# Kernel optimization log

Hardware: AMD Instinct MI355X
Metric: run time of the kernel (lower is better)

The kernel has to match this reference:

```python
import jax, jax.numpy as jnp
import numpy as np

ALPHA = 0.9

def setup_inputs() -> dict:
    key = jax.random.key(0)
    inputs = jax.random.normal(key, (8, 4096, 1024), dtype=jnp.float32)
    return {"inputs": inputs}

def reference(inputs) -> jnp.ndarray:
    # FOFE: y_t = alpha * y_{t-1} + x_t, y_{-1} = 0, over time axis (axis=1, batch_first).
    # Linear recurrence with constant decay -> associative scan over pairs (a, b)
    # representing y -> a*y + b.
    x = inputs  # [B, T, D]
    a = jnp.full(x.shape, ALPHA, dtype=x.dtype)  # decay per step

    def combine(c1, c2):
        a1, b1 = c1
        a2, b2 = c2
        return (a1 * a2, b1 * a2 + b2)

    _, y = jax.lax.associative_scan(combine, (a, x), axis=1)
    return y  # [B, T, D]
```

## Files before the change

### kernel.cpp

```cpp
#include <hip/hip_runtime.h>


#define ALPHA 0.9f
#define T_DIM 4096
#define D_DIM 1024
#define CH    512
#define WARM  128
#define DB    256

__global__ __launch_bounds__(256)
void fofe_kernel(const float* __restrict__ x, float* __restrict__ y) {
    const int NDB = D_DIM / DB;
    const int NCH = T_DIM / CH;

    int blk = blockIdx.x;
    int db  = blk % NDB;
    int ch  = (blk / NDB) % NCH;
    int b   = blk / (NDB * NCH);

    int d  = db * DB + threadIdx.x;
    int t0 = ch * CH;
    int tstart = (t0 >= WARM) ? (t0 - WARM) : 0;

    const float* __restrict__ xp = x + ((size_t)b * T_DIM) * D_DIM + d;
    float*       __restrict__ yp = y + ((size_t)b * T_DIM) * D_DIM + d;

    float acc = 0.0f;

    #pragma unroll 16
    for (int t = tstart; t < t0; ++t) {
        acc = fmaf(acc, ALPHA, xp[(size_t)t * D_DIM]);
    }

    #pragma unroll 16
    for (int t = t0; t < t0 + CH; ++t) {
        acc = fmaf(acc, ALPHA, xp[(size_t)t * D_DIM]);
        yp[(size_t)t * D_DIM] = acc;
    }
}

extern "C" void kernel_launch(void* const* d_in, const int* in_sizes, int n_in,
                              void* d_out, int out_size, void* d_ws, size_t ws_size,
                              hipStream_t stream) {
    const float* x = (const float*)d_in[0];
    float* y = (float*)d_out;

    const int B = 8;
    const int grid = B * (T_DIM / CH) * (D_DIM / DB);
    fofe_kernel<<<grid, DB, 0, stream>>>(x, y);
}
```

Before: 53.74 us.

## Vectorize FOFE scan with float4 per thread and shorten chunks and warmup

Each thread now processes four adjacent channels with float4 loads and stores, and each block covers the full feature width. The time chunk shrinks from 512 to 128 steps and the warmup from 128 to 64 steps. The aim is more bytes in flight per thread and more independent recurrence chains. In exchange, the redundant warmup reads grow as a fraction of chunk length, and the shorter warmup leaves a truncation error of about 0.9^64 that may be near tolerance.

```diff
diff --git a/kernel.cpp b/kernel.cpp
--- a/kernel.cpp
+++ b/kernel.cpp
@@ -4,48 +4,54 @@
 #define ALPHA 0.9f
 #define T_DIM 4096
 #define D_DIM 1024
-#define CH    512
-#define WARM  128
-#define DB    256
+#define CH    128
+#define WARM  64
+#define D4    (D_DIM / 4)
 
 __global__ __launch_bounds__(256)
-void fofe_kernel(const float* __restrict__ x, float* __restrict__ y) {
-    const int NDB = D_DIM / DB;
+void fofe_kernel(const float4* __restrict__ x, float4* __restrict__ y) {
     const int NCH = T_DIM / CH;
+    int blk = blockIdx.x;
+    int ch  = blk % NCH;
+    int b   = blk / NCH;
 
-    int blk = blockIdx.x;
-    int db  = blk % NDB;
-    int ch  = (blk / NDB) % NCH;
-    int b   = blk / (NDB * NCH);
-
-    int d  = db * DB + threadIdx.x;
     int t0 = ch * CH;
     int tstart = (t0 >= WARM) ? (t0 - WARM) : 0;
 
-    const float* __restrict__ xp = x + ((size_t)b * T_DIM) * D_DIM + d;
-    float*       __restrict__ yp = y + ((size_t)b * T_DIM) * D_DIM + d;
+    size_t base = (size_t)b * T_DIM * D4 + threadIdx.x;
+    const float4* __restrict__ xp = x + base;
+    float4*       __restrict__ yp = y + base;
 
-    float acc = 0.0f;
+    float ax = 0.0f, ay = 0.0f, az = 0.0f, aw = 0.0f;
 
     #pragma unroll 16
     for (int t = tstart; t < t0; ++t) {
-        acc = fmaf(acc, ALPHA, xp[(size_t)t * D_DIM]);
+        float4 v = xp[(size_t)t * D4];
+        ax = fmaf(ax, ALPHA, v.x);
+        ay = fmaf(ay, ALPHA, v.y);
+        az = fmaf(az, ALPHA, v.z);
+        aw = fmaf(aw, ALPHA, v.w);
     }
 
     #pragma unroll 16
     for (int t = t0; t < t0 + CH; ++t) {
-        acc = fmaf(acc, ALPHA, xp[(size_t)t * D_DIM]);
-        yp[(size_t)t * D_DIM] = acc;
+        float4 v = xp[(size_t)t * D4];
+        ax = fmaf(ax, ALPHA, v.x);
+        ay = fmaf(ay, ALPHA, v.y);
+        az = fmaf(az, ALPHA, v.z);
+        aw = fmaf(aw, ALPHA, v.w);
+        float4 o; o.x = ax; o.y = ay; o.z = az; o.w = aw;
+        yp[(size_t)t * D4] = o;
     }
 }
 
 extern "C" void kernel_launch(void* const* d_in, const int* in_sizes, int n_in,
                               void* d_out, int out_size, void* d_ws, size_t ws_size,
                               hipStream_t stream) {
-    const float* x = (const float*)d_in[0];
-    float* y = (float*)d_out;
+    const float4* x = (const float4*)d_in[0];
+    float4* y = (float4*)d_out;
 
     const int B = 8;
-    const int grid = B * (T_DIM / CH) * (D_DIM / DB);
-    fofe_kernel<<<grid, DB, 0, stream>>>(x, y);
+    const int grid = B * (T_DIM / CH);
+    fofe_kernel<<<grid, D4, 0, stream>>>(x, y);
 }
```

After: 53.75 us. Within noise of the previous version (+0.0%).
